# Kernel optimization log

Hardware: AMD Instinct MI355X
Metric: run time of the kernel (lower is better)

The kernel has to match this reference:

```python
import jax, jax.numpy as jnp
import numpy as np

N_HEADS = 16
LOCAL_WINDOW = 512
MAX_REL_DIST = 128
NEG_INF = jnp.float32(-1e30)


def setup_inputs() -> dict:
    key = jax.random.key(0)
    ks = jax.random.split(key, 5)
    B, T, C = 2, 2048, 1024
    x = jax.random.normal(ks[0], (B, T, C), dtype=jnp.float32)
    w_qkv = jax.random.normal(ks[1], (3 * C, C), dtype=jnp.float32) * 0.02
    w_proj = jax.random.normal(ks[2], (C, C), dtype=jnp.float32) * 0.02
    b_proj = jax.random.normal(ks[3], (C,), dtype=jnp.float32) * 0.02
    rel_bias = jax.random.normal(ks[4], (2 * MAX_REL_DIST + 1, N_HEADS), dtype=jnp.float32) * 0.02
    return {"x": x, "w_qkv": w_qkv, "w_proj": w_proj, "b_proj": b_proj, "rel_bias": rel_bias}


def reference(x, w_qkv, w_proj, b_proj, rel_bias):
    B, T, C = x.shape
    H = N_HEADS
    hd = C // H
    scale = hd ** -0.5
    # qkv projection: (B,T,3C) -> (3,B,H,T,hd)
    qkv = (x @ w_qkv.T).reshape(B, T, 3, H, hd).transpose(2, 0, 3, 1, 4)
    q, k, v = qkv[0], qkv[1], qkv[2]
    # full TxT scores (faithful to eager original)
    attn = jnp.einsum('bhqd,bhkd->bhqk', q, k) * scale
    i = jnp.arange(T)[:, None]
    j = jnp.arange(T)[None, :]
    mask = (i >= j) & (jnp.abs(i - j) <= LOCAL_WINDOW)
    attn = jnp.where(mask[None, None], attn, NEG_INF)
    # relative position bias: (H,T,T)
    rel = jnp.clip(i - j, -MAX_REL_DIST, MAX_REL_DIST) + MAX_REL_DIST
    bias = rel_bias[rel].transpose(2, 0, 1)  # (H,T,T)
    attn = attn + bias[None]
    attn = jax.nn.softmax(attn, axis=-1)
    y = jnp.einsum('bhqk,bhkd->bhqd', attn, v)
    y = y.transpose(0, 2, 1, 3).reshape(B, T, C)
    y = y @ w_proj.T + b_proj
    return y
```

## Files before the change

kernel.cpp:

```cpp
#include <hip/hip_runtime.h>

#define T_SEQ 2048
#define HD 64

typedef float f32x4 __attribute__((ext_vector_type(4)));
typedef __bf16 bf16x8 __attribute__((ext_vector_type(8)));
typedef unsigned short ushort8v __attribute__((ext_vector_type(8)));

__device__ __forceinline__ unsigned short f2bf(float f) {
    unsigned u = __builtin_bit_cast(unsigned, f);
    u += 0x7fffu + ((u >> 16) & 1u);
    return (unsigned short)(u >> 16);
}

__device__ __forceinline__ void gll16(const void* g, void* lds) {
    __builtin_amdgcn_global_load_lds(
        (const __attribute__((address_space(1))) unsigned int*)g,
        (__attribute__((address_space(3))) unsigned int*)lds, 16, 0, 0);
}

__device__ __forceinline__ bf16x8 ldfrag(const unsigned short* p) {
    return __builtin_bit_cast(bf16x8, *reinterpret_cast<const ushort8v*>(p));
}

__global__ __launch_bounds__(256)
void cvt_kernel(const float* __restrict__ s, unsigned short* __restrict__ d) {
    int i = (blockIdx.x * 256 + threadIdx.x) * 8;
    f32x4 a = *reinterpret_cast<const f32x4*>(s + i);
    f32x4 b = *reinterpret_cast<const f32x4*>(s + i + 4);
    ushort8v o;
#pragma unroll
    for (int j = 0; j < 4; ++j) { o[j] = f2bf(a[j]); o[4 + j] = f2bf(b[j]); }
    *reinterpret_cast<ushort8v*>(d + i) = o;
}

template<int MODE>
__global__ __launch_bounds__(256)
void gemm_kernel(const unsigned short* __restrict__ A, const unsigned short* __restrict__ W,
                 float* __restrict__ o0, unsigned short* __restrict__ qo,
                 unsigned short* __restrict__ ko, unsigned short* __restrict__ vo,
                 const float* __restrict__ bias)
{
    constexpr int K = 1024;
    __shared__ unsigned short As[128 * 32];
    __shared__ unsigned short Bs[128 * 32];
    const int t = threadIdx.x;
    const int m0 = blockIdx.x * 128, n0 = blockIdx.y * 128;
    const int lane = t & 63, w = t >> 6;
    const int wy = w >> 1, wx = w & 1;
    const int l15 = lane & 15, quad = lane >> 4;

    f32x4 acc[4][4] = {};
    const char* Ab = (const char*)A;
    const char* Wb = (const char*)W;

    for (int kc = 0; kc < K; kc += 32) {
#pragma unroll
        for (int i = 0; i < 2; ++i) {
            int c = w * 2 + i;
            int lin = c * 1024 + lane * 16;
            int row = lin >> 6, colb = lin & 63;
            gll16(Ab + ((size_t)(n0 + row) * K + kc) * 2 + colb, (char*)As + c * 1024);
            gll16(Wb + ((size_t)(m0 + row) * K + kc) * 2 + colb, (char*)Bs + c * 1024);
        }
        __syncthreads();
        bf16x8 af[4], bfr[4];
#pragma unroll
        for (int nt = 0; nt < 4; ++nt)
            af[nt] = ldfrag(As + (wy * 64 + nt * 16 + l15) * 32 + quad * 8);
#pragma unroll
        for (int mt = 0; mt < 4; ++mt)
            bfr[mt] = ldfrag(Bs + (wx * 64 + mt * 16 + l15) * 32 + quad * 8);
#pragma unroll
        for (int nt = 0; nt < 4; ++nt)
#pragma unroll
            for (int mt = 0; mt < 4; ++mt)
                acc[nt][mt] = __builtin_amdgcn_mfma_f32_16x16x32_bf16(af[nt], bfr[mt], acc[nt][mt], 0, 0, 0);
        __syncthreads();
    }

#pragma unroll
    for (int nt = 0; nt < 4; ++nt) {
#pragma unroll
        for (int mt = 0; mt < 4; ++mt) {
            const int m = m0 + wx * 64 + mt * 16 + l15;
#pragma unroll
            for (int r = 0; r < 4; ++r) {
                const int n = n0 + wy * 64 + nt * 16 + quad * 4 + r;
                float val = acc[nt][mt][r];
                if (MODE == 0) {
                    int bb = n >> 11, tt = n & 2047;
                    int s = m >> 10, h = (m >> 6) & 15, d = m & 63;
                    unsigned short* dst = (s == 0) ? qo : ((s == 1) ? ko : vo);
                    dst[((size_t)((bb << 4) + h) * T_SEQ + tt) * HD + d] = f2bf(val);
                } else {
                    o0[(size_t)n * 1024 + m] = val + bias[m];
                }
            }
        }
    }
}

__global__ __launch_bounds__(256)
void attn_kernel(const unsigned short* __restrict__ qg, const unsigned short* __restrict__ kg,
                 const unsigned short* __restrict__ vg, const float* __restrict__ rel_bias,
                 unsigned short* __restrict__ y)
{
    __shared__ unsigned short Ks[2 * 64 * 32];
    __shared__ unsigned short Vt[2 * 64 * 40];
    __shared__ unsigned short Pw[4 * 2 * 16 * 40];
    __shared__ float bias_s[260];

    const int t = threadIdx.x;
    const int lane = t & 63, w = t >> 6;
    const int l15 = lane & 15, quad = lane >> 4;
    const int qt = blockIdx.x, bh = blockIdx.y;
    const int b = bh >> 4, h = bh & 15;
    const int q0 = qt << 6;
    const size_t base = (size_t)bh * T_SEQ * HD;

    for (int i = t; i < 257; i += 256) bias_s[i] = rel_bias[i * 16 + h];

    bf16x8 qf[2];
#pragma unroll
    for (int ks = 0; ks < 2; ++ks)
        qf[ks] = ldfrag(qg + base + (size_t)(q0 + w * 16 + l15) * HD + ks * 32 + quad * 8);

    float m_r[4], l_r[4];
#pragma unroll
    for (int r = 0; r < 4; ++r) { m_r[r] = -1e30f; l_r[r] = 0.f; }
    f32x4 Oacc[4] = {};

    const int ig = q0 + w * 16 + quad * 4;
    unsigned short* Pme = Pw + w * (2 * 16 * 40);
    const int kt0 = (qt > 8) ? (qt - 8) : 0;

    for (int kt = kt0; kt <= qt; ++kt) {
        const char* kb = (const char*)(kg + base + (size_t)kt * 64 * HD);
#pragma unroll
        for (int i = 0; i < 2; ++i) {
            int c = w * 2 + i;
            int lin = c * 1024 + lane * 16;
            int ks = lin >> 12, rem = lin & 4095;
            int row = rem >> 6, colb = rem & 63;
            gll16(kb + row * 128 + ks * 64 + colb, (char*)Ks + c * 1024);
        }
        {
            const unsigned short* vb = vg + base + (size_t)kt * 64 * HD;
#pragma unroll
            for (int i = 0; i < 2; ++i) {
                int g = t + i * 256;
                int row = g >> 3, cg = (g & 7) * 8;
                ushort8v vv = *reinterpret_cast<const ushort8v*>(vb + row * 64 + cg);
                int ksb = row >> 5, kk = row & 31;
#pragma unroll
                for (int j = 0; j < 8; ++j) {
                    int c = cg + j;
                    int kk2 = kk ^ (((c >> 3) & 3) << 3);
                    Vt[ksb * (64 * 40) + c * 40 + kk2] = vv[j];
                }
            }
        }
        __syncthreads();

        f32x4 Sacc[4] = {};
#pragma unroll
        for (int ks = 0; ks < 2; ++ks)
#pragma unroll
            for (int ct = 0; ct < 4; ++ct) {
                bf16x8 kf = ldfrag(Ks + ks * 2048 + (ct * 16 + l15) * 32 + quad * 8);
                Sacc[ct] = __builtin_amdgcn_mfma_f32_16x16x32_bf16(qf[ks], kf, Sacc[ct], 0, 0, 0);
            }

        float sv[4][4];
#pragma unroll
        for (int ct = 0; ct < 4; ++ct) {
            int jg = (kt << 6) + ct * 16 + l15;
#pragma unroll
            for (int r = 0; r < 4; ++r) {
                int diff = ig + r - jg;
                sv[ct][r] = (diff < 0 || diff > 512) ? -1e30f
                          : Sacc[ct][r] * 0.125f + bias_s[(diff < 128 ? diff : 128) + 128];
            }
        }
        float mx[4];
#pragma unroll
        for (int r = 0; r < 4; ++r)
            mx[r] = fmaxf(fmaxf(sv[0][r], sv[1][r]), fmaxf(sv[2][r], sv[3][r]));
#pragma unroll
        for (int off = 1; off < 16; off <<= 1)
#pragma unroll
            for (int r = 0; r < 4; ++r) mx[r] = fmaxf(mx[r], __shfl_xor(mx[r], off, 64));
        float alpha[4];
#pragma unroll
        for (int r = 0; r < 4; ++r) {
            float mn = fmaxf(m_r[r], mx[r]);
            alpha[r] = __expf(m_r[r] - mn);
            m_r[r] = mn;
        }
        float ps[4] = {0.f, 0.f, 0.f, 0.f};
#pragma unroll
        for (int ct = 0; ct < 4; ++ct)
#pragma unroll
            for (int r = 0; r < 4; ++r) {
                float p = __expf(sv[ct][r] - m_r[r]);
                ps[r] += p;
                Pme[(ct >> 1) * (16 * 40) + (quad * 4 + r) * 40 + (ct & 1) * 16 + l15] = f2bf(p);
            }
#pragma unroll
        for (int off = 1; off < 16; off <<= 1)
#pragma unroll
            for (int r = 0; r < 4; ++r) ps[r] += __shfl_xor(ps[r], off, 64);
#pragma unroll
        for (int r = 0; r < 4; ++r) l_r[r] = l_r[r] * alpha[r] + ps[r];
#pragma unroll
        for (int ct2 = 0; ct2 < 4; ++ct2)
#pragma unroll
            for (int r = 0; r < 4; ++r) Oacc[ct2][r] *= alpha[r];
#pragma unroll
        for (int ks = 0; ks < 2; ++ks) {
            bf16x8 pf = ldfrag(Pme + ks * (16 * 40) + l15 * 40 + quad * 8);
#pragma unroll
            for (int ct2 = 0; ct2 < 4; ++ct2) {
                int n = ct2 * 16 + l15;
                int quadv = quad ^ ((n >> 3) & 3);
                bf16x8 vf = ldfrag(Vt + ks * (64 * 40) + n * 40 + quadv * 8);
                Oacc[ct2] = __builtin_amdgcn_mfma_f32_16x16x32_bf16(pf, vf, Oacc[ct2], 0, 0, 0);
            }
        }
        __syncthreads();
    }

    float inv[4];
#pragma unroll
    for (int r = 0; r < 4; ++r) inv[r] = 1.0f / l_r[r];
#pragma unroll
    for (int ct2 = 0; ct2 < 4; ++ct2)
#pragma unroll
        for (int r = 0; r < 4; ++r)
            y[((size_t)b * T_SEQ + q0 + w * 16 + quad * 4 + r) * 1024 + h * 64 + ct2 * 16 + l15]
                = f2bf(Oacc[ct2][r] * inv[r]);
}

extern "C" void kernel_launch(void* const* d_in, const int* in_sizes, int n_in,
                              void* d_out, int out_size, void* d_ws, size_t ws_size,
                              hipStream_t stream)
{
    (void)in_sizes; (void)n_in; (void)out_size; (void)ws_size;
    const float* x        = (const float*)d_in[0];
    const float* w_qkv    = (const float*)d_in[1];
    const float* w_proj   = (const float*)d_in[2];
    const float* b_proj   = (const float*)d_in[3];
    const float* rel_bias = (const float*)d_in[4];
    float* out = (float*)d_out;

    unsigned short* ws = (unsigned short*)d_ws;
    unsigned short* xb     = ws;
    unsigned short* wqkvb  = xb + 4194304;
    unsigned short* wprojb = wqkvb + 3145728;
    unsigned short* qb     = wprojb + 1048576;
    unsigned short* kb     = qb + 4194304;
    unsigned short* vb     = kb + 4194304;
    unsigned short* yab    = vb + 4194304;

    cvt_kernel<<<2048, 256, 0, stream>>>(x, xb);
    cvt_kernel<<<1536, 256, 0, stream>>>(w_qkv, wqkvb);
    cvt_kernel<<<512, 256, 0, stream>>>(w_proj, wprojb);
    gemm_kernel<0><<<dim3(24, 32), 256, 0, stream>>>(xb, wqkvb, nullptr, qb, kb, vb, nullptr);
    attn_kernel<<<dim3(32, 32), 256, 0, stream>>>(qb, kb, vb, rel_bias, yab);
    gemm_kernel<1><<<dim3(8, 32), 256, 0, stream>>>(yab, wprojb, out, nullptr, nullptr, nullptr, b_proj);
}
```

Baseline: 187.9 us.

## Restructure pipeline: fuse conversions, pre-transpose V, swizzle LDS, widen attention blocks

The three fp32-to-bf16 conversion launches become one kernel. The QKV GEMM now folds the softmax scale into Q, writes V already transposed, and uses XOR-swizzled LDS to avoid bank conflicts. Attention blocks now cover 128 queries with 8 waves and compute transposed scores so each lane owns one query row, which replaces the 16-lane shuffle reductions with two shuffles. Tiles outside the window are skipped, and the per-element bias and mask are dropped where the bias is constant. The projection GEMM moves to 512 threads with smaller per-wave tiles. The rewrite removes the scalar V transpose scatter into LDS, but idle waves on skipped tiles still wait at the barriers.

```diff
diff --git a/kernel.cpp b/kernel.cpp
--- a/kernel.cpp
+++ b/kernel.cpp
@@ -5,6 +5,7 @@
 
 typedef float f32x4 __attribute__((ext_vector_type(4)));
 typedef __bf16 bf16x8 __attribute__((ext_vector_type(8)));
+typedef unsigned short ushort4v __attribute__((ext_vector_type(4)));
 typedef unsigned short ushort8v __attribute__((ext_vector_type(8)));
 
 __device__ __forceinline__ unsigned short f2bf(float f) {
@@ -24,8 +25,16 @@
 }
 
 __global__ __launch_bounds__(256)
-void cvt_kernel(const float* __restrict__ s, unsigned short* __restrict__ d) {
-    int i = (blockIdx.x * 256 + threadIdx.x) * 8;
+void cvt_all_kernel(const float* __restrict__ x, const float* __restrict__ wq,
+                    const float* __restrict__ wp, unsigned short* __restrict__ xb,
+                    unsigned short* __restrict__ wqb, unsigned short* __restrict__ wpb)
+{
+    int bid = blockIdx.x;
+    const float* s; unsigned short* d; int off;
+    if (bid < 2048)      { s = x;  d = xb;  off = bid; }
+    else if (bid < 3584) { s = wq; d = wqb; off = bid - 2048; }
+    else                 { s = wp; d = wpb; off = bid - 3584; }
+    int i = (off * 256 + threadIdx.x) * 8;
     f32x4 a = *reinterpret_cast<const f32x4*>(s + i);
     f32x4 b = *reinterpret_cast<const f32x4*>(s + i + 4);
     ushort8v o;
@@ -34,12 +43,10 @@
     *reinterpret_cast<ushort8v*>(d + i) = o;
 }
 
-template<int MODE>
 __global__ __launch_bounds__(256)
-void gemm_kernel(const unsigned short* __restrict__ A, const unsigned short* __restrict__ W,
-                 float* __restrict__ o0, unsigned short* __restrict__ qo,
-                 unsigned short* __restrict__ ko, unsigned short* __restrict__ vo,
-                 const float* __restrict__ bias)
+void gemm_qkv_kernel(const unsigned short* __restrict__ A, const unsigned short* __restrict__ W,
+                     unsigned short* __restrict__ qo, unsigned short* __restrict__ ko,
+                     unsigned short* __restrict__ vo)
 {
     constexpr int K = 1024;
     __shared__ unsigned short As[128 * 32];
@@ -54,23 +61,24 @@
     const char* Ab = (const char*)A;
     const char* Wb = (const char*)W;
 
-    for (int kc = 0; kc < K; kc += 32) {
+    for (int kcl = 0; kcl < K; kcl += 32) {
 #pragma unroll
         for (int i = 0; i < 2; ++i) {
             int c = w * 2 + i;
             int lin = c * 1024 + lane * 16;
-            int row = lin >> 6, colb = lin & 63;
-            gll16(Ab + ((size_t)(n0 + row) * K + kc) * 2 + colb, (char*)As + c * 1024);
-            gll16(Wb + ((size_t)(m0 + row) * K + kc) * 2 + colb, (char*)Bs + c * 1024);
+            int row = lin >> 6;
+            int kc = ((lin & 63) >> 4) ^ (row & 3);
+            gll16(Ab + ((size_t)(n0 + row) * K + kcl + kc * 8) * 2, (char*)As + c * 1024);
+            gll16(Wb + ((size_t)(m0 + row) * K + kcl + kc * 8) * 2, (char*)Bs + c * 1024);
         }
         __syncthreads();
         bf16x8 af[4], bfr[4];
 #pragma unroll
         for (int nt = 0; nt < 4; ++nt)
-            af[nt] = ldfrag(As + (wy * 64 + nt * 16 + l15) * 32 + quad * 8);
+            af[nt] = ldfrag(As + (wy * 64 + nt * 16 + l15) * 32 + ((quad ^ (l15 & 3)) * 8));
 #pragma unroll
         for (int mt = 0; mt < 4; ++mt)
-            bfr[mt] = ldfrag(Bs + (wx * 64 + mt * 16 + l15) * 32 + quad * 8);
+            bfr[mt] = ldfrag(Bs + (wx * 64 + mt * 16 + l15) * 32 + ((quad ^ (l15 & 3)) * 8));
 #pragma unroll
         for (int nt = 0; nt < 4; ++nt)
 #pragma unroll
@@ -84,31 +92,83 @@
 #pragma unroll
         for (int mt = 0; mt < 4; ++mt) {
             const int m = m0 + wx * 64 + mt * 16 + l15;
+            const int s = m >> 10, h = (m >> 6) & 15, d = m & 63;
 #pragma unroll
             for (int r = 0; r < 4; ++r) {
                 const int n = n0 + wy * 64 + nt * 16 + quad * 4 + r;
+                const int bb = n >> 11, tt = n & 2047;
                 float val = acc[nt][mt][r];
-                if (MODE == 0) {
-                    int bb = n >> 11, tt = n & 2047;
-                    int s = m >> 10, h = (m >> 6) & 15, d = m & 63;
-                    unsigned short* dst = (s == 0) ? qo : ((s == 1) ? ko : vo);
-                    dst[((size_t)((bb << 4) + h) * T_SEQ + tt) * HD + d] = f2bf(val);
-                } else {
-                    o0[(size_t)n * 1024 + m] = val + bias[m];
-                }
+                if (s == 0)
+                    qo[((size_t)((bb << 4) + h) * T_SEQ + tt) * HD + d] = f2bf(val * 0.125f);
+                else if (s == 1)
+                    ko[((size_t)((bb << 4) + h) * T_SEQ + tt) * HD + d] = f2bf(val);
+                else
+                    vo[((size_t)((bb << 4) + h) * HD + d) * T_SEQ + tt] = f2bf(val);
             }
         }
     }
 }
 
-__global__ __launch_bounds__(256)
+__global__ __launch_bounds__(512, 4)
+void gemm_proj_kernel(const unsigned short* __restrict__ A, const unsigned short* __restrict__ W,
+                      float* __restrict__ o0, const float* __restrict__ bias)
+{
+    constexpr int K = 1024;
+    __shared__ unsigned short As[128 * 32];
+    __shared__ unsigned short Bs[128 * 32];
+    const int t = threadIdx.x;
+    const int m0 = blockIdx.x * 128, n0 = blockIdx.y * 128;
+    const int lane = t & 63, w = t >> 6;
+    const int wy = w >> 1, wx = w & 1;
+    const int l15 = lane & 15, quad = lane >> 4;
+
+    f32x4 acc[2][4] = {};
+    const char* Ab = (const char*)A;
+    const char* Wb = (const char*)W;
+    const int srow = t >> 2;
+    const int skc = (t & 3) ^ (srow & 3);
+
+    for (int kcl = 0; kcl < K; kcl += 32) {
+        gll16(Ab + ((size_t)(n0 + srow) * K + kcl + skc * 8) * 2, (char*)As + w * 1024);
+        gll16(Wb + ((size_t)(m0 + srow) * K + kcl + skc * 8) * 2, (char*)Bs + w * 1024);
+        __syncthreads();
+        bf16x8 af[2], bfr[4];
+#pragma unroll
+        for (int nt = 0; nt < 2; ++nt)
+            af[nt] = ldfrag(As + (wy * 32 + nt * 16 + l15) * 32 + ((quad ^ (l15 & 3)) * 8));
+#pragma unroll
+        for (int mt = 0; mt < 4; ++mt)
+            bfr[mt] = ldfrag(Bs + (wx * 64 + mt * 16 + l15) * 32 + ((quad ^ (l15 & 3)) * 8));
+#pragma unroll
+        for (int nt = 0; nt < 2; ++nt)
+#pragma unroll
+            for (int mt = 0; mt < 4; ++mt)
+                acc[nt][mt] = __builtin_amdgcn_mfma_f32_16x16x32_bf16(af[nt], bfr[mt], acc[nt][mt], 0, 0, 0);
+        __syncthreads();
+    }
+
+#pragma unroll
+    for (int nt = 0; nt < 2; ++nt)
+#pragma unroll
+        for (int mt = 0; mt < 4; ++mt) {
+            const int m = m0 + wx * 64 + mt * 16 + l15;
+            const float bm = bias[m];
+#pragma unroll
+            for (int r = 0; r < 4; ++r) {
+                const int n = n0 + wy * 32 + nt * 16 + quad * 4 + r;
+                o0[(size_t)n * 1024 + m] = acc[nt][mt][r] + bm;
+            }
+        }
+}
+
+__global__ __launch_bounds__(512, 4)
 void attn_kernel(const unsigned short* __restrict__ qg, const unsigned short* __restrict__ kg,
-                 const unsigned short* __restrict__ vg, const float* __restrict__ rel_bias,
+                 const unsigned short* __restrict__ vt, const float* __restrict__ rel_bias,
                  unsigned short* __restrict__ y)
 {
-    __shared__ unsigned short Ks[2 * 64 * 32];
-    __shared__ unsigned short Vt[2 * 64 * 40];
-    __shared__ unsigned short Pw[4 * 2 * 16 * 40];
+    __shared__ unsigned short Ks[64 * 64];
+    __shared__ unsigned short Vt[64 * 64];
+    __shared__ unsigned short Pl[8 * 16 * 72];
     __shared__ float bias_s[260];
 
     const int t = threadIdx.x;
@@ -116,130 +176,114 @@
     const int l15 = lane & 15, quad = lane >> 4;
     const int qt = blockIdx.x, bh = blockIdx.y;
     const int b = bh >> 4, h = bh & 15;
-    const int q0 = qt << 6;
+    const int q0 = qt << 7;
+    const int qw0 = q0 + w * 16;
+    const int q_row = qw0 + l15;
     const size_t base = (size_t)bh * T_SEQ * HD;
 
-    for (int i = t; i < 257; i += 256) bias_s[i] = rel_bias[i * 16 + h];
+    for (int i = t; i < 257; i += 512) bias_s[i] = rel_bias[i * 16 + h];
 
     bf16x8 qf[2];
 #pragma unroll
     for (int ks = 0; ks < 2; ++ks)
-        qf[ks] = ldfrag(qg + base + (size_t)(q0 + w * 16 + l15) * HD + ks * 32 + quad * 8);
-
-    float m_r[4], l_r[4];
-#pragma unroll
-    for (int r = 0; r < 4; ++r) { m_r[r] = -1e30f; l_r[r] = 0.f; }
+        qf[ks] = ldfrag(qg + base + (size_t)q_row * HD + ks * 32 + quad * 8);
+
+    float m_r = -1e30f, l_r = 0.f;
     f32x4 Oacc[4] = {};
 
-    const int ig = q0 + w * 16 + quad * 4;
-    unsigned short* Pme = Pw + w * (2 * 16 * 40);
-    const int kt0 = (qt > 8) ? (qt - 8) : 0;
-
-    for (int kt = kt0; kt <= qt; ++kt) {
-        const char* kb = (const char*)(kg + base + (size_t)kt * 64 * HD);
-#pragma unroll
-        for (int i = 0; i < 2; ++i) {
-            int c = w * 2 + i;
-            int lin = c * 1024 + lane * 16;
-            int ks = lin >> 12, rem = lin & 4095;
-            int row = rem >> 6, colb = rem & 63;
-            gll16(kb + row * 128 + ks * 64 + colb, (char*)Ks + c * 1024);
+    unsigned short* Pme = Pl + w * (16 * 72);
+    const int srow = t >> 3;
+    const int skc = (t & 7) ^ (srow & 7);
+
+    const int kt0 = (qt * 2 > 8) ? (qt * 2 - 8) : 0;
+    const int kt1 = qt * 2 + 1;
+
+    for (int kt = kt0; kt <= kt1; ++kt) {
+        gll16((const char*)(kg + base + (size_t)(kt * 64 + srow) * HD + skc * 8), (char*)Ks + w * 1024);
+        gll16((const char*)(vt + base + (size_t)srow * T_SEQ + kt * 64 + skc * 8), (char*)Vt + w * 1024);
+        __syncthreads();
+
+        const int delta = qw0 - kt * 64;
+        if (delta >= 0 && delta <= 560) {
+            f32x4 Sacc[4] = {};
+#pragma unroll
+            for (int ks = 0; ks < 2; ++ks)
+#pragma unroll
+                for (int ct = 0; ct < 4; ++ct) {
+                    bf16x8 kf = ldfrag(Ks + (ct * 16 + l15) * 64 + (((ks * 4 + quad) ^ (l15 & 7)) * 8));
+                    Sacc[ct] = __builtin_amdgcn_mfma_f32_16x16x32_bf16(kf, qf[ks], Sacc[ct], 0, 0, 0);
+                }
+
+            float sv[4][4];
+            if (delta >= 192 && delta <= 496) {
+                const float bC = bias_s[256];
+#pragma unroll
+                for (int ct = 0; ct < 4; ++ct)
+#pragma unroll
+                    for (int r = 0; r < 4; ++r) sv[ct][r] = Sacc[ct][r] + bC;
+            } else {
+#pragma unroll
+                for (int ct = 0; ct < 4; ++ct)
+#pragma unroll
+                    for (int r = 0; r < 4; ++r) {
+                        int diff = q_row - (kt * 64 + ct * 16 + quad * 4 + r);
+                        float bb = bias_s[(diff < 128 ? diff : 128) + 128];
+                        float s = Sacc[ct][r] + bb;
+                        sv[ct][r] = (diff < 0 || diff > 512) ? -1e30f : s;
+                    }
+            }
+
+            float mx = -1e30f;
+#pragma unroll
+            for (int ct = 0; ct < 4; ++ct)
+#pragma unroll
+                for (int r = 0; r < 4; ++r) mx = fmaxf(mx, sv[ct][r]);
+            mx = fmaxf(mx, __shfl_xor(mx, 16, 64));
+            mx = fmaxf(mx, __shfl_xor(mx, 32, 64));
+            float mn = fmaxf(m_r, mx);
+            float alpha = __expf(m_r - mn);
+            m_r = mn;
+            float ps = 0.f;
+            float p[4][4];
+#pragma unroll
+            for (int ct = 0; ct < 4; ++ct)
+#pragma unroll
+                for (int r = 0; r < 4; ++r) { p[ct][r] = __expf(sv[ct][r] - mn); ps += p[ct][r]; }
+            ps += __shfl_xor(ps, 16, 64);
+            ps += __shfl_xor(ps, 32, 64);
+            l_r = l_r * alpha + ps;
+
+#pragma unroll
+            for (int ct = 0; ct < 4; ++ct) {
+                ushort4v pw;
+#pragma unroll
+                for (int j = 0; j < 4; ++j) pw[j] = f2bf(p[ct][j]);
+                *reinterpret_cast<ushort4v*>(Pme + l15 * 72 + ct * 16 + quad * 4) = pw;
+            }
+#pragma unroll
+            for (int mt = 0; mt < 4; ++mt) Oacc[mt] *= alpha;
+#pragma unroll
+            for (int ks = 0; ks < 2; ++ks) {
+                bf16x8 pf = ldfrag(Pme + l15 * 72 + ks * 32 + quad * 8);
+#pragma unroll
+                for (int mt = 0; mt < 4; ++mt) {
+                    bf16x8 vf = ldfrag(Vt + (mt * 16 + l15) * 64 + (((ks * 4 + quad) ^ (l15 & 7)) * 8));
+                    Oacc[mt] = __builtin_amdgcn_mfma_f32_16x16x32_bf16(vf, pf, Oacc[mt], 0, 0, 0);
+                }
+            }
         }
-        {
-            const unsigned short* vb = vg + base + (size_t)kt * 64 * HD;
-#pragma unroll
-            for (int i = 0; i < 2; ++i) {
-                int g = t + i * 256;
-                int row = g >> 3, cg = (g & 7) * 8;
-                ushort8v vv = *reinterpret_cast<const ushort8v*>(vb + row * 64 + cg);
-                int ksb = row >> 5, kk = row & 31;
-#pragma unroll
-                for (int j = 0; j < 8; ++j) {
-                    int c = cg + j;
-                    int kk2 = kk ^ (((c >> 3) & 3) << 3);
-                    Vt[ksb * (64 * 40) + c * 40 + kk2] = vv[j];
-                }
-            }
-        }
-        __syncthreads();
-
-        f32x4 Sacc[4] = {};
-#pragma unroll
-        for (int ks = 0; ks < 2; ++ks)
-#pragma unroll
-            for (int ct = 0; ct < 4; ++ct) {
-                bf16x8 kf = ldfrag(Ks + ks * 2048 + (ct * 16 + l15) * 32 + quad * 8);
-                Sacc[ct] = __builtin_amdgcn_mfma_f32_16x16x32_bf16(qf[ks], kf, Sacc[ct], 0, 0, 0);
-            }
-
-        float sv[4][4];
-#pragma unroll
-        for (int ct = 0; ct < 4; ++ct) {
-            int jg = (kt << 6) + ct * 16 + l15;
-#pragma unroll
-            for (int r = 0; r < 4; ++r) {
-                int diff = ig + r - jg;
-                sv[ct][r] = (diff < 0 || diff > 512) ? -1e30f
-                          : Sacc[ct][r] * 0.125f + bias_s[(diff < 128 ? diff : 128) + 128];
-            }
-        }
-        float mx[4];
-#pragma unroll
-        for (int r = 0; r < 4; ++r)
-            mx[r] = fmaxf(fmaxf(sv[0][r], sv[1][r]), fmaxf(sv[2][r], sv[3][r]));
-#pragma unroll
-        for (int off = 1; off < 16; off <<= 1)
-#pragma unroll
-            for (int r = 0; r < 4; ++r) mx[r] = fmaxf(mx[r], __shfl_xor(mx[r], off, 64));
-        float alpha[4];
-#pragma unroll
-        for (int r = 0; r < 4; ++r) {
-            float mn = fmaxf(m_r[r], mx[r]);
-            alpha[r] = __expf(m_r[r] - mn);
-            m_r[r] = mn;
-        }
-        float ps[4] = {0.f, 0.f, 0.f, 0.f};
-#pragma unroll
-        for (int ct = 0; ct < 4; ++ct)
-#pragma unroll
-            for (int r = 0; r < 4; ++r) {
-                float p = __expf(sv[ct][r] - m_r[r]);
-                ps[r] += p;
-                Pme[(ct >> 1) * (16 * 40) + (quad * 4 + r) * 40 + (ct & 1) * 16 + l15] = f2bf(p);
-            }
-#pragma unroll
-        for (int off = 1; off < 16; off <<= 1)
-#pragma unroll
-            for (int r = 0; r < 4; ++r) ps[r] += __shfl_xor(ps[r], off, 64);
-#pragma unroll
-        for (int r = 0; r < 4; ++r) l_r[r] = l_r[r] * alpha[r] + ps[r];
-#pragma unroll
-        for (int ct2 = 0; ct2 < 4; ++ct2)
-#pragma unroll
-            for (int r = 0; r < 4; ++r) Oacc[ct2][r] *= alpha[r];
-#pragma unroll
-        for (int ks = 0; ks < 2; ++ks) {
-            bf16x8 pf = ldfrag(Pme + ks * (16 * 40) + l15 * 40 + quad * 8);
-#pragma unroll
-            for (int ct2 = 0; ct2 < 4; ++ct2) {
-                int n = ct2 * 16 + l15;
-                int quadv = quad ^ ((n >> 3) & 3);
-                bf16x8 vf = ldfrag(Vt + ks * (64 * 40) + n * 40 + quadv * 8);
-                Oacc[ct2] = __builtin_amdgcn_mfma_f32_16x16x32_bf16(pf, vf, Oacc[ct2], 0, 0, 0);
-            }
-        }
-        __syncthreads();
-    }
-
-    float inv[4];
-#pragma unroll
-    for (int r = 0; r < 4; ++r) inv[r] = 1.0f / l_r[r];
-#pragma unroll
-    for (int ct2 = 0; ct2 < 4; ++ct2)
-#pragma unroll
-        for (int r = 0; r < 4; ++r)
-            y[((size_t)b * T_SEQ + q0 + w * 16 + quad * 4 + r) * 1024 + h * 64 + ct2 * 16 + l15]
-                = f2bf(Oacc[ct2][r] * inv[r]);
+        __syncthreads();
+    }
+
+    const float inv = 1.0f / l_r;
+    unsigned short* yp = y + ((size_t)b * T_SEQ + q_row) * 1024 + h * 64;
+#pragma unroll
+    for (int mt = 0; mt < 4; ++mt) {
+        ushort4v o;
+#pragma unroll
+        for (int j = 0; j < 4; ++j) o[j] = f2bf(Oacc[mt][j] * inv);
+        *reinterpret_cast<ushort4v*>(yp + mt * 16 + quad * 4) = o;
+    }
 }
 
 extern "C" void kernel_launch(void* const* d_in, const int* in_sizes, int n_in,
@@ -260,13 +304,11 @@
     unsigned short* wprojb = wqkvb + 3145728;
     unsigned short* qb     = wprojb + 1048576;
     unsigned short* kb     = qb + 4194304;
-    unsigned short* vb     = kb + 4194304;
-    unsigned short* yab    = vb + 4194304;
-
-    cvt_kernel<<<2048, 256, 0, stream>>>(x, xb);
-    cvt_kernel<<<1536, 256, 0, stream>>>(w_qkv, wqkvb);
-    cvt_kernel<<<512, 256, 0, stream>>>(w_proj, wprojb);
-    gemm_kernel<0><<<dim3(24, 32), 256, 0, stream>>>(xb, wqkvb, nullptr, qb, kb, vb, nullptr);
-    attn_kernel<<<dim3(32, 32), 256, 0, stream>>>(qb, kb, vb, rel_bias, yab);
-    gemm_kernel<1><<<dim3(8, 32), 256, 0, stream>>>(yab, wprojb, out, nullptr, nullptr, nullptr, b_proj);
-}
+    unsigned short* vtb    = kb + 4194304;
+    unsigned short* yab    = vtb + 4194304;
+
+    cvt_all_kernel<<<4096, 256, 0, stream>>>(x, w_qkv, w_proj, xb, wqkvb, wprojb);
+    gemm_qkv_kernel<<<dim3(24, 32), 256, 0, stream>>>(xb, wqkvb, qb, kb, vtb);
+    attn_kernel<<<dim3(16, 32), 512, 0, stream>>>(qb, kb, vtb, rel_bias, yab);
+    gemm_proj_kernel<<<dim3(8, 32), 512, 0, stream>>>(yab, wprojb, out, b_proj);
+}
```

New measurement: 176.8 us. 5.9% less time.
